# Kernel tuning notes

Hardware: AMD Instinct MI355X
Metric: run time of the kernel (lower is better)

Reference implementation:

```python
import jax, jax.numpy as jnp
import numpy as np

B, S, D, H, FF = 2, 1024, 1024, 16, 4096
EPS = 1e-6  # flax LayerNorm default


def _layernorm(x, scale, bias):
    m = jnp.mean(x, axis=-1, keepdims=True)
    v = jnp.mean(jnp.square(x - m), axis=-1, keepdims=True)
    return (x - m) * jax.lax.rsqrt(v + EPS) * scale + bias


def _attention(x, mask, w_qkv, b_qkv, w_o, b_o):
    # projection to 3*D, split into q,k,v
    p = x @ w_qkv + b_qkv                       # (B,S,3D)
    q, k, v = jnp.split(p, 3, axis=-1)          # each (B,S,D)
    hd = D // H
    # NOTE: faithful to source -- heads formed by a plain reshape of (B,S,D)
    qh = q.reshape(B, H, S, hd)
    kh = k.reshape(B, H, S, hd)
    vh = v.reshape(B, H, S, hd)
    # NOTE: scaled by sqrt(full hidden dim D), as in source (dim_key = key.shape[-1])
    scores = jnp.einsum('bhqd,bhkd->bhqk', qh, kh) / jnp.sqrt(jnp.asarray(D, x.dtype))
    scores = scores * mask                      # multiplicative mask (faithful)
    attn = jax.nn.softmax(scores, axis=-1)      # (B,H,S,S)
    ctx = jnp.einsum('bhqk,bhkd->bhqd', attn, vh).reshape(B, S, D)
    return ctx @ w_o + b_o, attn


def _geglu_ffn(x, w1, b1, wg, bg, w2, b2):
    h = x @ w1 + b1                              # (B,S,FF)
    g = h @ wg + bg                              # (B,S,2*FF)
    a, gate = g[..., :FF], g[..., FF:]
    tanh_res = jnp.tanh(gate * 0.7978845608 * (1 + 0.044715 * gate ** 2))
    act = a * 0.5 * gate * (1 + tanh_res)
    return act @ w2 + b2


def setup_inputs() -> dict:
    key = jax.random.key(0)
    ks = jax.random.split(key, 16)
    sc = 0.02
    inp = {
        'x': jax.random.normal(ks[0], (B, S, D), jnp.float32),
        'ln1_s': jnp.ones((D,), jnp.float32), 'ln1_b': jnp.zeros((D,), jnp.float32),
        'w_qkv1': jax.random.normal(ks[1], (D, 3 * D), jnp.float32) * sc,
        'b_qkv1': jnp.zeros((3 * D,), jnp.float32),
        'w_o1': jax.random.normal(ks[2], (D, D), jnp.float32) * sc,
        'b_o1': jnp.zeros((D,), jnp.float32),
        'ln2_s': jnp.ones((D,), jnp.float32), 'ln2_b': jnp.zeros((D,), jnp.float32),
        'w_qkv2': jax.random.normal(ks[3], (D, 3 * D), jnp.float32) * sc,
        'b_qkv2': jnp.zeros((3 * D,), jnp.float32),
        'w_o2': jax.random.normal(ks[4], (D, D), jnp.float32) * sc,
        'b_o2': jnp.zeros((D,), jnp.float32),
        'ln3_s': jnp.ones((D,), jnp.float32), 'ln3_b': jnp.zeros((D,), jnp.float32),
        'w1': jax.random.normal(ks[5], (D, FF), jnp.float32) * sc,
        'b1': jnp.zeros((FF,), jnp.float32),
        'wg': jax.random.normal(ks[6], (FF, 2 * FF), jnp.float32) * sc,
        'bg': jnp.zeros((2 * FF,), jnp.float32),
        'w2': jax.random.normal(ks[7], (FF, D), jnp.float32) * sc,
        'b2': jnp.zeros((D,), jnp.float32),
    }
    return inp


def reference(x, ln1_s, ln1_b, w_qkv1, b_qkv1, w_o1, b_o1,
              ln2_s, ln2_b, w_qkv2, b_qkv2, w_o2, b_o2,
              ln3_s, ln3_b, w1, b1, wg, bg, w2, b2):
    # causal mask: lower-triangular ones, multiplicative, broadcast over (B,H)
    mask = (jnp.arange(S)[:, None] >= jnp.arange(S)[None, :]).astype(jnp.int32)
    mask = jnp.broadcast_to(mask[None, None], (B, H, S, S))

    x = _layernorm(x, ln1_s, ln1_b)
    att1, attn_w1 = _attention(x, mask, w_qkv1, b_qkv1, w_o1, b_o1)
    x = x + att1                                  # dropout deterministic (identity)
    x = _layernorm(x, ln2_s, ln2_b)
    att2, attn_w2 = _attention(x, mask, w_qkv2, b_qkv2, w_o2, b_o2)
    x = x + att2
    x = _layernorm(x, ln3_s, ln3_b)
    out = _geglu_ffn(x, w1, b1, wg, bg, w2, b2)
    # NOTE: faithful to source -- final residual adds attention2 output
    x = out + att2
    return (x, attn_w1, attn_w2)
```

## Files before the change

### kernel.cpp

```cpp
#include <hip/hip_runtime.h>
#include <hip/hip_bf16.h>

#define B_ 2
#define S_ 1024
#define D_ 1024
#define H_ 16
#define HD_ 64
#define FF_ 4096
#define NROW_ (B_*S_)

typedef __hip_bfloat16 bf16;
typedef float f32x4 __attribute__((ext_vector_type(4)));
typedef int int4v __attribute__((ext_vector_type(4)));
typedef __bf16 bf16x8 __attribute__((ext_vector_type(8)));

__device__ __forceinline__ float bf2f(unsigned short u){
  return __uint_as_float((unsigned)u << 16);
}
__device__ __forceinline__ unsigned short f2bf(float f){
  unsigned u = __float_as_uint(f);
  return (unsigned short)((u + 0x7FFFu + ((u >> 16) & 1u)) >> 16);
}
__device__ __forceinline__ float gelu_gate(float a, float g){
  float t = tanhf(0.7978845608f * g * (1.f + 0.044715f * g * g));
  return a * 0.5f * g * (1.f + t);
}


__global__ __launch_bounds__(256) void tcvt(const float* __restrict__ W,
    unsigned short* __restrict__ Wt, int K, int N){
  __shared__ float tile[32][33];
  const int k0 = blockIdx.y*32, n0 = blockIdx.x*32;
  const int t = threadIdx.x;
  #pragma unroll
  for (int i = 0; i < 4; i++){
    int idx = t + i*256; int r = idx>>5, c = idx&31;
    tile[r][c] = W[(size_t)(k0+r)*N + n0 + c];
  }
  __syncthreads();
  #pragma unroll
  for (int i = 0; i < 4; i++){
    int idx = t + i*256; int r = idx>>5, c = idx&31;
    Wt[(size_t)(n0+r)*K + k0 + c] = f2bf(tile[c][r]);
  }
}

__global__ __launch_bounds__(256) void lnb_k(const float* __restrict__ x,
    const float* __restrict__ sc, const float* __restrict__ bi, unsigned short* __restrict__ y){
  const int row = blockIdx.x;
  const int t = threadIdx.x;
  const float* xr = x + (size_t)row * D_;
  float4 v = *(const float4*)&xr[t*4];
  __shared__ float red[8];
  float sum = v.x + v.y + v.z + v.w;
  #pragma unroll
  for (int o = 32; o > 0; o >>= 1) sum += __shfl_down(sum, o);
  if ((t & 63) == 0) red[t >> 6] = sum;
  __syncthreads();
  if (t == 0) red[4] = (red[0]+red[1]+red[2]+red[3]) * (1.f / D_);
  __syncthreads();
  const float mean = red[4];
  const float dx = v.x-mean, dy = v.y-mean, dz = v.z-mean, dw = v.w-mean;
  float sq = dx*dx + dy*dy + dz*dz + dw*dw;
  #pragma unroll
  for (int o = 32; o > 0; o >>= 1) sq += __shfl_down(sq, o);
  if ((t & 63) == 0) red[t >> 6] = sq;
  __syncthreads();
  if (t == 0) red[5] = (red[0]+red[1]+red[2]+red[3]) * (1.f / D_);
  __syncthreads();
  const float rstd = rsqrtf(red[5] + 1e-6f);
  float4 s4 = *(const float4*)&sc[t*4];
  float4 b4 = *(const float4*)&bi[t*4];
  ushort4 ov;
  ov.x = f2bf(dx*rstd*s4.x + b4.x);
  ov.y = f2bf(dy*rstd*s4.y + b4.y);
  ov.z = f2bf(dz*rstd*s4.z + b4.z);
  ov.w = f2bf(dw*rstd*s4.w + b4.w);
  *(ushort4*)&y[(size_t)row*D_ + t*4] = ov;
}

template<bool HAS_RES, bool RES_BF16, bool OUT_BF16>
__global__ __launch_bounds__(256) void mgemm(const unsigned short* __restrict__ A,
    const unsigned short* __restrict__ Bt, const float* __restrict__ bias,
    const void* __restrict__ res, void* __restrict__ Cv, int M, int N, int K){
  __shared__ unsigned short As[128*32];
  __shared__ unsigned short Bs[128*32];
  const int tid = threadIdx.x;
  const int bm = blockIdx.y*128, bn = blockIdx.x*128;
  const int lane = tid & 63, lq = lane >> 4, lr = lane & 15;
  const int wv = tid >> 6, wr = wv >> 1, wc = wv & 1;
  f32x4 acc[4][4] = {};
  int4v ra[2], rb[2];
  #pragma unroll
  for (int i = 0; i < 2; i++){
    int f = tid + i*256; int row = f>>2, s = f&3;
    ra[i] = *(const int4v*)&A[(size_t)(bm+row)*K + s*8];
    rb[i] = *(const int4v*)&Bt[(size_t)(bn+row)*K + s*8];
  }
  for (int k0 = 0; k0 < K; k0 += 32){
    __syncthreads();
    #pragma unroll
    for (int i = 0; i < 2; i++){
      int f = tid + i*256; int row = f>>2, s = f&3;
      int off = row*32 + ((s + (row>>1))&3)*8;
      *(int4v*)&As[off] = ra[i];
      *(int4v*)&Bs[off] = rb[i];
    }
    __syncthreads();
    if (k0 + 32 < K){
      #pragma unroll
      for (int i = 0; i < 2; i++){
        int f = tid + i*256; int row = f>>2, s = f&3;
        ra[i] = *(const int4v*)&A[(size_t)(bm+row)*K + k0+32 + s*8];
        rb[i] = *(const int4v*)&Bt[(size_t)(bn+row)*K + k0+32 + s*8];
      }
    }
    bf16x8 af[4], bfr[4];
    #pragma unroll
    for (int fm = 0; fm < 4; fm++){
      int r = wr*64 + fm*16 + lr;
      af[fm] = *(const bf16x8*)&As[r*32 + ((lq + (r>>1))&3)*8];
    }
    #pragma unroll
    for (int fn = 0; fn < 4; fn++){
      int r = wc*64 + fn*16 + lr;
      bfr[fn] = *(const bf16x8*)&Bs[r*32 + ((lq + (r>>1))&3)*8];
    }
    #pragma unroll
    for (int fm = 0; fm < 4; fm++)
      #pragma unroll
      for (int fn = 0; fn < 4; fn++)
        acc[fm][fn] = __builtin_amdgcn_mfma_f32_16x16x32_bf16(af[fm], bfr[fn], acc[fm][fn], 0, 0, 0);
  }
  #pragma unroll
  for (int fm = 0; fm < 4; fm++)
    #pragma unroll
    for (int fn = 0; fn < 4; fn++)
      #pragma unroll
      for (int rr = 0; rr < 4; rr++){
        int r = bm + wr*64 + fm*16 + lq*4 + rr;
        int c = bn + wc*64 + fn*16 + lr;
        size_t o = (size_t)r*N + c;
        float v = acc[fm][fn][rr] + bias[c];
        if (HAS_RES){
          if (RES_BF16) v += bf2f(((const unsigned short*)res)[o]);
          else          v += ((const float*)res)[o];
        }
        if (OUT_BF16) ((unsigned short*)Cv)[o] = f2bf(v);
        else          ((float*)Cv)[o] = v;
      }
}

__global__ __launch_bounds__(256) void mqkv(const unsigned short* __restrict__ A,
    const unsigned short* __restrict__ Bt, const float* __restrict__ bias,
    unsigned short* __restrict__ qh, unsigned short* __restrict__ kh, unsigned short* __restrict__ vt){
  const int K = D_;
  __shared__ unsigned short As[128*32];
  __shared__ unsigned short Bs[128*32];
  const int tid = threadIdx.x;
  const int bm = blockIdx.y*128, bn = blockIdx.x*128;
  const int lane = tid & 63, lq = lane >> 4, lr = lane & 15;
  const int wv = tid >> 6, wr = wv >> 1, wc = wv & 1;
  f32x4 acc[4][4] = {};
  int4v ra[2], rb[2];
  #pragma unroll
  for (int i = 0; i < 2; i++){
    int f = tid + i*256; int row = f>>2, s = f&3;
    ra[i] = *(const int4v*)&A[(size_t)(bm+row)*K + s*8];
    rb[i] = *(const int4v*)&Bt[(size_t)(bn+row)*K + s*8];
  }
  for (int k0 = 0; k0 < K; k0 += 32){
    __syncthreads();
    #pragma unroll
    for (int i = 0; i < 2; i++){
      int f = tid + i*256; int row = f>>2, s = f&3;
      int off = row*32 + ((s + (row>>1))&3)*8;
      *(int4v*)&As[off] = ra[i];
      *(int4v*)&Bs[off] = rb[i];
    }
    __syncthreads();
    if (k0 + 32 < K){
      #pragma unroll
      for (int i = 0; i < 2; i++){
        int f = tid + i*256; int row = f>>2, s = f&3;
        ra[i] = *(const int4v*)&A[(size_t)(bm+row)*K + k0+32 + s*8];
        rb[i] = *(const int4v*)&Bt[(size_t)(bn+row)*K + k0+32 + s*8];
      }
    }
    bf16x8 af[4], bfr[4];
    #pragma unroll
    for (int fm = 0; fm < 4; fm++){
      int r = wr*64 + fm*16 + lr;
      af[fm] = *(const bf16x8*)&As[r*32 + ((lq + (r>>1))&3)*8];
    }
    #pragma unroll
    for (int fn = 0; fn < 4; fn++){
      int r = wc*64 + fn*16 + lr;
      bfr[fn] = *(const bf16x8*)&Bs[r*32 + ((lq + (r>>1))&3)*8];
    }
    #pragma unroll
    for (int fm = 0; fm < 4; fm++)
      #pragma unroll
      for (int fn = 0; fn < 4; fn++)
        acc[fm][fn] = __builtin_amdgcn_mfma_f32_16x16x32_bf16(af[fm], bfr[fn], acc[fm][fn], 0, 0, 0);
  }
  #pragma unroll
  for (int fm = 0; fm < 4; fm++)
    #pragma unroll
    for (int fn = 0; fn < 4; fn++){
      int cbase = bn + wc*64 + fn*16 + lr;
      float bv = bias[cbase];
      if (cbase < 2*D_){
        unsigned short* dst = (cbase < D_) ? qh : kh;
        int cc = cbase & (D_-1);
        int u = cc >> 6, d2 = cc & 63;
        #pragma unroll
        for (int rr = 0; rr < 4; rr++){
          int r = bm + wr*64 + fm*16 + lq*4 + rr;
          int b = r >> 10, s = r & (S_-1);
          int h = s >> 6;
          int s2 = ((s & 63) << 4) + u;
          size_t off = (((size_t)(b*H_ + h))*S_ + s2)*HD_ + d2;
          dst[off] = f2bf(acc[fm][fn][rr] + bv);
        }
      } else {
        int cc = cbase - 2*D_;
        int u = cc >> 6, d2 = cc & 63;
        #pragma unroll
        for (int rr = 0; rr < 4; rr++){
          int r = bm + wr*64 + fm*16 + lq*4 + rr;
          int b = r >> 10, s = r & (S_-1);
          int h = s >> 6;
          int s2 = ((s & 63) << 4) + u;
          size_t off = (((size_t)(b*H_ + h))*HD_ + d2)*S_ + s2;
          vt[off] = f2bf(acc[fm][fn][rr] + bv);
        }
      }
    }
}

__global__ __launch_bounds__(256) void mgeglu(const unsigned short* __restrict__ A,
    const unsigned short* __restrict__ Wt, const float* __restrict__ bgp, unsigned short* __restrict__ act){
  const int K = FF_;
  __shared__ unsigned short As[128*32];
  __shared__ unsigned short Ba[64*32];
  __shared__ unsigned short Bg[64*32];
  const int tid = threadIdx.x;
  const int bm = blockIdx.y*128, bn = blockIdx.x*64;
  const int lane = tid & 63, lq = lane >> 4, lr = lane & 15;
  const int wv = tid >> 6, wr = wv >> 1, wc = wv & 1;
  f32x4 aa[4][2] = {};
  f32x4 ag[4][2] = {};
  int4v ra[2], rba, rbg;
  #pragma unroll
  for (int i = 0; i < 2; i++){
    int f = tid + i*256; int row = f>>2, s = f&3;
    ra[i] = *(const int4v*)&A[(size_t)(bm+row)*K + s*8];
  }
  { int row = tid>>2, s = tid&3;
    rba = *(const int4v*)&Wt[(size_t)(bn+row)*K + s*8];
    rbg = *(const int4v*)&Wt[(size_t)(FF_+bn+row)*K + s*8];
  }
  for (int k0 = 0; k0 < K; k0 += 32){
    __syncthreads();
    #pragma unroll
    for (int i = 0; i < 2; i++){
      int f = tid + i*256; int row = f>>2, s = f&3;
      *(int4v*)&As[row*32 + ((s + (row>>1))&3)*8] = ra[i];
    }
    { int row = tid>>2, s = tid&3;
      int off = row*32 + ((s + (row>>1))&3)*8;
      *(int4v*)&Ba[off] = rba;
      *(int4v*)&Bg[off] = rbg;
    }
    __syncthreads();
    if (k0 + 32 < K){
      #pragma unroll
      for (int i = 0; i < 2; i++){
        int f = tid + i*256; int row = f>>2, s = f&3;
        ra[i] = *(const int4v*)&A[(size_t)(bm+row)*K + k0+32 + s*8];
      }
      { int row = tid>>2, s = tid&3;
        rba = *(const int4v*)&Wt[(size_t)(bn+row)*K + k0+32 + s*8];
        rbg = *(const int4v*)&Wt[(size_t)(FF_+bn+row)*K + k0+32 + s*8];
      }
    }
    bf16x8 af[4], fa[2], fg[2];
    #pragma unroll
    for (int fm = 0; fm < 4; fm++){
      int r = wr*64 + fm*16 + lr;
      af[fm] = *(const bf16x8*)&As[r*32 + ((lq + (r>>1))&3)*8];
    }
    #pragma unroll
    for (int fn = 0; fn < 2; fn++){
      int r = wc*32 + fn*16 + lr;
      int off = r*32 + ((lq + (r>>1))&3)*8;
      fa[fn] = *(const bf16x8*)&Ba[off];
      fg[fn] = *(const bf16x8*)&Bg[off];
    }
    #pragma unroll
    for (int fm = 0; fm < 4; fm++)
      #pragma unroll
      for (int fn = 0; fn < 2; fn++){
        aa[fm][fn] = __builtin_amdgcn_mfma_f32_16x16x32_bf16(af[fm], fa[fn], aa[fm][fn], 0, 0, 0);
        ag[fm][fn] = __builtin_amdgcn_mfma_f32_16x16x32_bf16(af[fm], fg[fn], ag[fm][fn], 0, 0, 0);
      }
  }
  #pragma unroll
  for (int fm = 0; fm < 4; fm++)
    #pragma unroll
    for (int fn = 0; fn < 2; fn++)
      #pragma unroll
      for (int rr = 0; rr < 4; rr++){
        int r = bm + wr*64 + fm*16 + lq*4 + rr;
        int c = bn + wc*32 + fn*16 + lr;
        float a = aa[fm][fn][rr] + bgp[c];
        float g = ag[fm][fn][rr] + bgp[FF_ + c];
        act[(size_t)r*FF_ + c] = f2bf(gelu_gate(a, g));
      }
}

__global__ __launch_bounds__(256) void mstats(const unsigned short* __restrict__ qh,
    const unsigned short* __restrict__ kh, float2* __restrict__ stats){
  const int qt = blockIdx.x, bh = blockIdx.y;
  const int tid = threadIdx.x;
  const int lane = tid & 63, lq = lane >> 4, lr = lane & 15;
  const int wv = tid >> 6, wr = wv >> 1, wc = wv & 1;
  __shared__ unsigned short Qs[128*64];
  __shared__ unsigned short Ks[128*64];
  __shared__ float2 st[2][2][64];
  const unsigned short* Qp = qh + ((size_t)bh*S_ + qt*128)*HD_;
  #pragma unroll
  for (int i = 0; i < 4; i++){
    int f = tid + i*256;
    int row = f >> 3, s = f & 7;
    *(int4v*)&Qs[row*64 + ((s + row)&7)*8] = *(const int4v*)&Qp[(size_t)row*HD_ + s*8];
  }
  float m[4][4], l[4][4];
  #pragma unroll
  for (int fm = 0; fm < 4; fm++)
    #pragma unroll
    for (int rr = 0; rr < 4; rr++){ m[fm][rr] = -3.4e38f; l[fm][rr] = 0.f; }
  const int qg0 = qt*128;
  for (int kt = 0; kt <= qt; kt++){
    __syncthreads();
    const unsigned short* Kp = kh + ((size_t)bh*S_ + kt*128)*HD_;
    #pragma unroll
    for (int i = 0; i < 4; i++){
      int f = tid + i*256;
      int row = f >> 3, s = f & 7;
      *(int4v*)&Ks[row*64 + ((s + row)&7)*8] = *(const int4v*)&Kp[(size_t)row*HD_ + s*8];
    }
    __syncthreads();
    f32x4 acc[4][4] = {};
    #pragma unroll
    for (int ks = 0; ks < 2; ks++){
      bf16x8 af[4], bfr[4];
      #pragma unroll
      for (int fm = 0; fm < 4; fm++){
        int r = wr*64 + fm*16 + lr;
        af[fm] = *(const bf16x8*)&Qs[r*64 + ((ks*4+lq + r)&7)*8];
      }
      #pragma unroll
      for (int fn = 0; fn < 4; fn++){
        int r = wc*64 + fn*16 + lr;
        bfr[fn] = *(const bf16x8*)&Ks[r*64 + ((ks*4+lq + r)&7)*8];
      }
      #pragma unroll
      for (int fm = 0; fm < 4; fm++)
        #pragma unroll
        for (int fn = 0; fn < 4; fn++)
          acc[fm][fn] = __builtin_amdgcn_mfma_f32_16x16x32_bf16(af[fm], bfr[fn], acc[fm][fn], 0, 0, 0);
    }
    const int kg0 = kt*128;
    #pragma unroll
    for (int fm = 0; fm < 4; fm++)
      #pragma unroll
      for (int rr = 0; rr < 4; rr++){
        int r = wr*64 + fm*16 + lq*4 + rr;
        float v0 = (kg0 + wc*64 +  0 + lr <= qg0 + r) ? acc[fm][0][rr]*(1.f/32.f) : 0.f;
        float v1 = (kg0 + wc*64 + 16 + lr <= qg0 + r) ? acc[fm][1][rr]*(1.f/32.f) : 0.f;
        float v2 = (kg0 + wc*64 + 32 + lr <= qg0 + r) ? acc[fm][2][rr]*(1.f/32.f) : 0.f;
        float v3 = (kg0 + wc*64 + 48 + lr <= qg0 + r) ? acc[fm][3][rr]*(1.f/32.f) : 0.f;
        float tmax = fmaxf(fmaxf(v0,v1), fmaxf(v2,v3));
        tmax = fmaxf(tmax, __shfl_xor(tmax,1));
        tmax = fmaxf(tmax, __shfl_xor(tmax,2));
        tmax = fmaxf(tmax, __shfl_xor(tmax,4));
        tmax = fmaxf(tmax, __shfl_xor(tmax,8));
        float mn = fmaxf(m[fm][rr], tmax);
        float se = __expf(v0-mn)+__expf(v1-mn)+__expf(v2-mn)+__expf(v3-mn);
        se += __shfl_xor(se,1); se += __shfl_xor(se,2);
        se += __shfl_xor(se,4); se += __shfl_xor(se,8);
        l[fm][rr] = l[fm][rr]*__expf(m[fm][rr]-mn) + se;
        m[fm][rr] = mn;
      }
  }
  if (lr == 0){
    #pragma unroll
    for (int fm = 0; fm < 4; fm++)
      #pragma unroll
      for (int rr = 0; rr < 4; rr++){
        float2 v; v.x = m[fm][rr]; v.y = l[fm][rr];
        st[wr][wc][fm*16 + lq*4 + rr] = v;
      }
  }
  __syncthreads();
  if (wc == 0 && lr == 0){
    const float nz = (float)((7 - qt)*128);
    #pragma unroll
    for (int fm = 0; fm < 4; fm++)
      #pragma unroll
      for (int rr = 0; rr < 4; rr++){
        int r64 = fm*16 + lq*4 + rr;
        float2 a = st[wr][0][r64], b = st[wr][1][r64];
        float mf = fmaxf(a.x, b.x);
        float lf = a.y*__expf(a.x-mf) + b.y*__expf(b.x-mf);
        if (nz > 0.f){
          float mz = fmaxf(mf, 0.f);
          lf = lf*__expf(mf-mz) + nz*__expf(-mz);
          mf = mz;
        }
        float2 o; o.x = mf; o.y = lf;
        stats[(size_t)bh*S_ + qt*128 + wr*64 + r64] = o;
      }
  }
}

__global__ __launch_bounds__(256) void mpv(const unsigned short* __restrict__ qh,
    const unsigned short* __restrict__ kh, const unsigned short* __restrict__ vt,
    const float2* __restrict__ stats, float* __restrict__ attn, unsigned short* __restrict__ ctx){
  const int qt = blockIdx.x, bh = blockIdx.y;
  const int b = bh >> 4, h = bh & 15;
  const int tid = threadIdx.x;
  const int lane = tid & 63, lq = lane >> 4, lr = lane & 15;
  const int wv = tid >> 6, wr = wv >> 1, wc = wv & 1;
  __shared__ unsigned short Qs[128*64];
  __shared__ unsigned short Ks[128*64];
  __shared__ unsigned short Pt[128*128];
  __shared__ unsigned short Vt[64*128];
  const unsigned short* Qp = qh + ((size_t)bh*S_ + qt*128)*HD_;
  const unsigned short* Vp = vt + (size_t)bh*HD_*S_;
  float* Ap = attn + ((size_t)bh*S_ + qt*128)*S_;
  #pragma unroll
  for (int i = 0; i < 4; i++){
    int f = tid + i*256;
    int row = f >> 3, s = f & 7;
    *(int4v*)&Qs[row*64 + ((s + row)&7)*8] = *(const int4v*)&Qp[(size_t)row*HD_ + s*8];
  }
  float mS[4][4], lI[4][4];
  #pragma unroll
  for (int fm = 0; fm < 4; fm++)
    #pragma unroll
    for (int rr = 0; rr < 4; rr++){
      float2 s2 = stats[(size_t)bh*S_ + qt*128 + wr*64 + fm*16 + lq*4 + rr];
      mS[fm][rr] = s2.x; lI[fm][rr] = 1.f / s2.y;
    }
  const int qg0 = qt*128;
  f32x4 oacc[4][2] = {};
  for (int kt = 0; kt < 8; kt++){
    __syncthreads();
    #pragma unroll
    for (int i = 0; i < 4; i++){
      int f = tid + i*256;
      int row = f >> 4, s = f & 15;
      *(int4v*)&Vt[row*128 + ((s + row)&15)*8] = *(const int4v*)&Vp[(size_t)row*S_ + kt*128 + s*8];
    }
    if (kt <= qt){
      const unsigned short* Kp = kh + ((size_t)bh*S_ + kt*128)*HD_;
      #pragma unroll
      for (int i = 0; i < 4; i++){
        int f = tid + i*256;
        int row = f >> 3, s = f & 7;
        *(int4v*)&Ks[row*64 + ((s + row)&7)*8] = *(const int4v*)&Kp[(size_t)row*HD_ + s*8];
      }
      __syncthreads();
      f32x4 acc[4][4] = {};
      #pragma unroll
      for (int ks = 0; ks < 2; ks++){
        bf16x8 af[4], bfr[4];
        #pragma unroll
        for (int fm = 0; fm < 4; fm++){
          int r = wr*64 + fm*16 + lr;
          af[fm] = *(const bf16x8*)&Qs[r*64 + ((ks*4+lq + r)&7)*8];
        }
        #pragma unroll
        for (int fn = 0; fn < 4; fn++){
          int r = wc*64 + fn*16 + lr;
          bfr[fn] = *(const bf16x8*)&Ks[r*64 + ((ks*4+lq + r)&7)*8];
        }
        #pragma unroll
        for (int fm = 0; fm < 4; fm++)
          #pragma unroll
          for (int fn = 0; fn < 4; fn++)
            acc[fm][fn] = __builtin_amdgcn_mfma_f32_16x16x32_bf16(af[fm], bfr[fn], acc[fm][fn], 0, 0, 0);
      }
      const int kg0 = kt*128;
      #pragma unroll
      for (int fm = 0; fm < 4; fm++)
        #pragma unroll
        for (int fn = 0; fn < 4; fn++)
          #pragma unroll
          for (int rr = 0; rr < 4; rr++){
            int r = wr*64 + fm*16 + lq*4 + rr;
            int c = wc*64 + fn*16 + lr;
            float v = (kg0 + c <= qg0 + r) ? acc[fm][fn][rr]*(1.f/32.f) : 0.f;
            float p = __expf(v - mS[fm][rr]) * lI[fm][rr];
            Ap[(size_t)r*S_ + kg0 + c] = p;
            Pt[r*128 + (((c>>3) + r)&15)*8 + (c&7)] = f2bf(p);
          }
      __syncthreads();
    } else {
      __syncthreads();
      int rt = tid >> 1, hk = tid & 1;
      float2 srow = stats[(size_t)bh*S_ + qt*128 + rt];
      float p = __expf(-srow.x) * (1.f / srow.y);
      unsigned short pb = f2bf(p);
      int rep = (unsigned)pb | ((unsigned)pb << 16);
      int4v pv = {rep, rep, rep, rep};
      float4 pf = {p, p, p, p};
      #pragma unroll
      for (int sl = 0; sl < 8; sl++){
        int slot = hk*8 + sl;
        *(int4v*)&Pt[rt*128 + ((slot + rt)&15)*8] = pv;
        *(float4*)&Ap[(size_t)rt*S_ + kt*128 + hk*64 + sl*8] = pf;
        *(float4*)&Ap[(size_t)rt*S_ + kt*128 + hk*64 + sl*8 + 4] = pf;
      }
      __syncthreads();
    }
    #pragma unroll
    for (int ks = 0; ks < 4; ks++){
      bf16x8 af[4], bfv[2];
      #pragma unroll
      for (int fm = 0; fm < 4; fm++){
        int r = wr*64 + fm*16 + lr;
        af[fm] = *(const bf16x8*)&Pt[r*128 + ((ks*4+lq + r)&15)*8];
      }
      #pragma unroll
      for (int fn = 0; fn < 2; fn++){
        int r = wc*32 + fn*16 + lr;
        bfv[fn] = *(const bf16x8*)&Vt[r*128 + ((ks*4+lq + r)&15)*8];
      }
      #pragma unroll
      for (int fm = 0; fm < 4; fm++)
        #pragma unroll
        for (int fn = 0; fn < 2; fn++)
          oacc[fm][fn] = __builtin_amdgcn_mfma_f32_16x16x32_bf16(af[fm], bfv[fn], oacc[fm][fn], 0, 0, 0);
    }
  }
  #pragma unroll
  for (int fm = 0; fm < 4; fm++)
    #pragma unroll
    for (int fn = 0; fn < 2; fn++){
      int d = wc*32 + fn*16 + lr;
      #pragma unroll
      for (int rr = 0; rr < 4; rr++){
        int q = qt*128 + wr*64 + fm*16 + lq*4 + rr;
        size_t orow = ((size_t)b*S_ + h*HD_ + (q>>4)) * D_ + ((q&15)<<6) + d;
        ctx[orow] = f2bf(oacc[fm][fn][rr]);
      }
    }
}

__global__ __launch_bounds__(256) void addbf(const unsigned short* __restrict__ a,
    const float* __restrict__ b, float* __restrict__ c){
  size_t i = ((size_t)blockIdx.x*256 + threadIdx.x)*4;
  ushort4 av = *(const ushort4*)&a[i];
  float4 bv = *(const float4*)&b[i];
  float4 o = {bf2f(av.x)+bv.x, bf2f(av.y)+bv.y, bf2f(av.z)+bv.z, bf2f(av.w)+bv.w};
  *(float4*)&c[i] = o;
}


__global__ __launch_bounds__(256) void ln_kernel(const float* __restrict__ x,
    const float* __restrict__ sc, const float* __restrict__ bi, float* __restrict__ y){
  const int row = blockIdx.x;
  const int t = threadIdx.x;
  const float* xr = x + (size_t)row * D_;
  float4 v = *(const float4*)&xr[t*4];
  __shared__ float red[8];
  float sum = v.x + v.y + v.z + v.w;
  #pragma unroll
  for (int o = 32; o > 0; o >>= 1) sum += __shfl_down(sum, o);
  if ((t & 63) == 0) red[t >> 6] = sum;
  __syncthreads();
  if (t == 0) red[4] = (red[0]+red[1]+red[2]+red[3]) * (1.f / D_);
  __syncthreads();
  const float mean = red[4];
  const float dx = v.x-mean, dy = v.y-mean, dz = v.z-mean, dw = v.w-mean;
  float sq = dx*dx + dy*dy + dz*dz + dw*dw;
  #pragma unroll
  for (int o = 32; o > 0; o >>= 1) sq += __shfl_down(sq, o);
  if ((t & 63) == 0) red[t >> 6] = sq;
  __syncthreads();
  if (t == 0) red[5] = (red[0]+red[1]+red[2]+red[3]) * (1.f / D_);
  __syncthreads();
  const float rstd = rsqrtf(red[5] + 1e-6f);
  float4 s4 = *(const float4*)&sc[t*4];
  float4 b4 = *(const float4*)&bi[t*4];
  float4 o4;
  o4.x = dx*rstd*s4.x + b4.x;
  o4.y = dy*rstd*s4.y + b4.y;
  o4.z = dz*rstd*s4.z + b4.z;
  o4.w = dw*rstd*s4.w + b4.w;
  *(float4*)&y[(size_t)row*D_ + t*4] = o4;
}

__global__ __launch_bounds__(256) void gemm_qkv_kernel(const float* __restrict__ A,
    const float* __restrict__ W, const float* __restrict__ bias,
    float* __restrict__ qh, float* __restrict__ kh, float* __restrict__ vh){
  constexpr int BK=32;
  const int K = D_, N = 3*D_;
  __shared__ float As[BK][64+4];
  __shared__ float Bs[BK][64+4];
  const int bm = blockIdx.y*64, bn = blockIdx.x*64;
  const int tid = threadIdx.x;
  const int tx = tid & 15, ty = tid >> 4;
  float acc[4][4] = {};
  for (int k0 = 0; k0 < K; k0 += BK){
    #pragma unroll
    for (int i = 0; i < 2; i++){
      int idx = tid + i*256;
      int m = idx >> 3, kq = idx & 7;
      float4 v = *(const float4*)&A[(size_t)(bm+m)*K + k0 + kq*4];
      As[kq*4+0][m] = v.x; As[kq*4+1][m] = v.y;
      As[kq*4+2][m] = v.z; As[kq*4+3][m] = v.w;
    }
    #pragma unroll
    for (int i = 0; i < 2; i++){
      int idx = tid + i*256;
      int k = idx >> 4, nq = idx & 15;
      *(float4*)&Bs[k][nq*4] = *(const float4*)&W[(size_t)(k0+k)*N + bn + nq*4];
    }
    __syncthreads();
    #pragma unroll
    for (int kk = 0; kk < BK; kk++){
      float4 a4 = *(const float4*)&As[kk][ty*4];
      float4 b4 = *(const float4*)&Bs[kk][tx*4];
      float a[4] = {a4.x,a4.y,a4.z,a4.w};
      float b[4] = {b4.x,b4.y,b4.z,b4.w};
      #pragma unroll
      for (int i = 0; i < 4; i++)
        #pragma unroll
        for (int j = 0; j < 4; j++)
          acc[i][j] += a[i]*b[j];
    }
    __syncthreads();
  }
  float4 bias4 = *(const float4*)&bias[bn + tx*4];
  float* dst = (bn < D_) ? qh : (bn < 2*D_) ? kh : vh;
  const int c = (bn & (D_-1)) + tx*4;
  const int u = c >> 6;
  const int d2 = c & 63;
  #pragma unroll
  for (int i = 0; i < 4; i++){
    int r = bm + ty*4 + i;
    int b = r >> 10, s = r & (S_-1);
    int h = s >> 6;
    int s2 = ((s & 63) << 4) + u;
    size_t off = (((size_t)(b*H_ + h))*S_ + s2)*HD_ + d2;
    float4 o = {acc[i][0]+bias4.x, acc[i][1]+bias4.y, acc[i][2]+bias4.z, acc[i][3]+bias4.w};
    *(float4*)&dst[off] = o;
  }
}

__global__ __launch_bounds__(256) void attn_kernel(const float* __restrict__ qh,
    const float* __restrict__ kh, float* __restrict__ attn){
  const int q = blockIdx.x & (S_-1);
  const int bh = blockIdx.x >> 10;
  const int t = threadIdx.x;
  const float* qrow = qh + ((size_t)bh*S_ + q) * HD_;
  const float* Kp = kh + (size_t)bh*S_*HD_;
  __shared__ float qs[HD_];
  __shared__ float red[8];
  if (t < 16) ((float4*)qs)[t] = ((const float4*)qrow)[t];
  __syncthreads();
  float vals[4];
  float vmax = 0.f;
  #pragma unroll
  for (int j = 0; j < 4; j++){
    int k = t + j*256;
    float dot = 0.f;
    if (k <= q){
      const float4* Kr = (const float4*)&Kp[(size_t)k*HD_];
      #pragma unroll
      for (int dqi = 0; dqi < 16; dqi++){
        float4 kv = Kr[dqi];
        float4 qv = ((const float4*)qs)[dqi];
        dot += kv.x*qv.x + kv.y*qv.y + kv.z*qv.z + kv.w*qv.w;
      }
      dot *= (1.f/32.f);
    }
    vals[j] = dot;
    vmax = fmaxf(vmax, dot);
  }
  #pragma unroll
  for (int o = 32; o > 0; o >>= 1) vmax = fmaxf(vmax, __shfl_down(vmax, o));
  if ((t & 63) == 0) red[t >> 6] = vmax;
  __syncthreads();
  if (t == 0) red[4] = fmaxf(fmaxf(red[0],red[1]), fmaxf(red[2],red[3]));
  __syncthreads();
  const float m = red[4];
  float lsum = 0.f;
  #pragma unroll
  for (int j = 0; j < 4; j++){ vals[j] = __expf(vals[j]-m); lsum += vals[j]; }
  #pragma unroll
  for (int o = 32; o > 0; o >>= 1) lsum += __shfl_down(lsum, o);
  if ((t & 63) == 0) red[t >> 6] = lsum;
  __syncthreads();
  if (t == 0) red[5] = red[0]+red[1]+red[2]+red[3];
  __syncthreads();
  const float rinv = 1.f / red[5];
  float* arow = attn + ((size_t)bh*S_ + q) * S_;
  #pragma unroll
  for (int j = 0; j < 4; j++)
    arow[t + j*256] = vals[j] * rinv;
}

__global__ __launch_bounds__(256) void ctx_kernel(const float* __restrict__ attn,
    const float* __restrict__ vh, float* __restrict__ ctx){
  constexpr int BQ = 64, BK = 32;
  __shared__ float As[BK][BQ+4];
  __shared__ float Bs[BK][HD_+4];
  const int bh = blockIdx.y;
  const int b = bh >> 4, h = bh & 15;
  const int q0 = blockIdx.x * BQ;
  const float* Ap = attn + (size_t)bh*S_*S_;
  const float* Vp = vh + (size_t)bh*S_*HD_;
  const int tid = threadIdx.x;
  const int tx = tid & 15, ty = tid >> 4;
  float acc[4][4] = {};
  for (int k0 = 0; k0 < S_; k0 += BK){
    #pragma unroll
    for (int i = 0; i < 2; i++){
      int idx = tid + i*256;
      int m = idx >> 3, kq = idx & 7;
      float4 v = *(const float4*)&Ap[(size_t)(q0+m)*S_ + k0 + kq*4];
      As[kq*4+0][m] = v.x; As[kq*4+1][m] = v.y;
      As[kq*4+2][m] = v.z; As[kq*4+3][m] = v.w;
    }
    #pragma unroll
    for (int i = 0; i < 2; i++){
      int idx = tid + i*256;
      int k = idx >> 4, nq = idx & 15;
      *(float4*)&Bs[k][nq*4] = *(const float4*)&Vp[(size_t)(k0+k)*HD_ + nq*4];
    }
    __syncthreads();
    #pragma unroll
    for (int kk = 0; kk < BK; kk++){
      float4 a4 = *(const float4*)&As[kk][ty*4];
      float4 b4 = *(const float4*)&Bs[kk][tx*4];
      float a[4] = {a4.x,a4.y,a4.z,a4.w};
      float bb[4] = {b4.x,b4.y,b4.z,b4.w};
      #pragma unroll
      for (int i=0;i<4;i++)
        #pragma unroll
        for (int j=0;j<4;j++)
          acc[i][j] += a[i]*bb[j];
    }
    __syncthreads();
  }
  #pragma unroll
  for (int i = 0; i < 4; i++){
    int qq = q0 + ty*4 + i;
    size_t orow = ((size_t)b*S_ + h*HD_ + (qq>>4)) * D_ + ((qq&15)<<6) + tx*4;
    float4 o4 = {acc[i][0], acc[i][1], acc[i][2], acc[i][3]};
    *(float4*)&ctx[orow] = o4;
  }
}

template<bool A_BF16>
__global__ __launch_bounds__(256) void gemm_kernel(const void* __restrict__ Av,
    const float* __restrict__ W, const float* __restrict__ bias,
    const float* __restrict__ res, float* __restrict__ C,
    int M, int N, int K){
  constexpr int BK=32;
  __shared__ float As[BK][64+4];
  __shared__ float Bs[BK][64+4];
  const int bm = blockIdx.y*64, bn = blockIdx.x*64;
  const int tid = threadIdx.x;
  const int tx = tid & 15, ty = tid >> 4;
  float acc[4][4] = {};
  for (int k0 = 0; k0 < K; k0 += BK){
    #pragma unroll
    for (int i = 0; i < 2; i++){
      int idx = tid + i*256;
      int m = idx >> 3, kq = idx & 7;
      if (A_BF16){
        const unsigned short* A = (const unsigned short*)Av;
        ushort4 uu = *(const ushort4*)&A[(size_t)(bm+m)*K + k0 + kq*4];
        As[kq*4+0][m] = bf2f(uu.x); As[kq*4+1][m] = bf2f(uu.y);
        As[kq*4+2][m] = bf2f(uu.z); As[kq*4+3][m] = bf2f(uu.w);
      } else {
        const float* A = (const float*)Av;
        float4 v = *(const float4*)&A[(size_t)(bm+m)*K + k0 + kq*4];
        As[kq*4+0][m] = v.x; As[kq*4+1][m] = v.y;
        As[kq*4+2][m] = v.z; As[kq*4+3][m] = v.w;
      }
    }
    #pragma unroll
    for (int i = 0; i < 2; i++){
      int idx = tid + i*256;
      int k = idx >> 4, nq = idx & 15;
      *(float4*)&Bs[k][nq*4] = *(const float4*)&W[(size_t)(k0+k)*N + bn + nq*4];
    }
    __syncthreads();
    #pragma unroll
    for (int kk = 0; kk < BK; kk++){
      float4 a4 = *(const float4*)&As[kk][ty*4];
      float4 b4 = *(const float4*)&Bs[kk][tx*4];
      float a[4] = {a4.x,a4.y,a4.z,a4.w};
      float b[4] = {b4.x,b4.y,b4.z,b4.w};
      #pragma unroll
      for (int i = 0; i < 4; i++)
        #pragma unroll
        for (int j = 0; j < 4; j++)
          acc[i][j] += a[i]*b[j];
    }
    __syncthreads();
  }
  float4 bias4 = *(const float4*)&bias[bn + tx*4];
  #pragma unroll
  for (int i = 0; i < 4; i++){
    int r = bm + ty*4 + i;
    size_t base = (size_t)r*N + bn + tx*4;
    float c0 = acc[i][0] + bias4.x;
    float c1 = acc[i][1] + bias4.y;
    float c2 = acc[i][2] + bias4.z;
    float c3 = acc[i][3] + bias4.w;
    if (res){
      float4 r4 = *(const float4*)&res[base];
      c0 += r4.x; c1 += r4.y; c2 += r4.z; c3 += r4.w;
    }
    float4 o4 = {c0,c1,c2,c3};
    *(float4*)&C[base] = o4;
  }
}

__global__ __launch_bounds__(256) void gemm_geglu_kernel(const float* __restrict__ A,
    const float* __restrict__ W, const float* __restrict__ bgp, unsigned short* __restrict__ act){
  constexpr int BK=32;
  const int K = FF_, N = 2*FF_;
  __shared__ float As[BK][64+4];
  __shared__ float Ba[BK][64+4];
  __shared__ float Bg[BK][64+4];
  const int bm = blockIdx.y*64, bn = blockIdx.x*64;
  const int tid = threadIdx.x;
  const int tx = tid & 15, ty = tid >> 4;
  float acc_a[4][4] = {};
  float acc_g[4][4] = {};
  for (int k0 = 0; k0 < K; k0 += BK){
    #pragma unroll
    for (int i = 0; i < 2; i++){
      int idx = tid + i*256;
      int m = idx >> 3, kq = idx & 7;
      float4 v = *(const float4*)&A[(size_t)(bm+m)*K + k0 + kq*4];
      As[kq*4+0][m] = v.x; As[kq*4+1][m] = v.y;
      As[kq*4+2][m] = v.z; As[kq*4+3][m] = v.w;
    }
    #pragma unroll
    for (int i = 0; i < 2; i++){
      int idx = tid + i*256;
      int k = idx >> 4, nq = idx & 15;
      const float* Wr = &W[(size_t)(k0+k)*N];
      *(float4*)&Ba[k][nq*4] = *(const float4*)&Wr[bn + nq*4];
      *(float4*)&Bg[k][nq*4] = *(const float4*)&Wr[FF_ + bn + nq*4];
    }
    __syncthreads();
    #pragma unroll
    for (int kk = 0; kk < BK; kk++){
      float4 a4 = *(const float4*)&As[kk][ty*4];
      float4 p4 = *(const float4*)&Ba[kk][tx*4];
      float4 g4 = *(const float4*)&Bg[kk][tx*4];
      float a[4] = {a4.x,a4.y,a4.z,a4.w};
      float pa[4] = {p4.x,p4.y,p4.z,p4.w};
      float pg[4] = {g4.x,g4.y,g4.z,g4.w};
      #pragma unroll
      for (int i = 0; i < 4; i++)
        #pragma unroll
        for (int j = 0; j < 4; j++){
          acc_a[i][j] += a[i]*pa[j];
          acc_g[i][j] += a[i]*pg[j];
        }
    }
    __syncthreads();
  }
  float4 ba4 = *(const float4*)&bgp[bn + tx*4];
  float4 bg4 = *(const float4*)&bgp[FF_ + bn + tx*4];
  const float bav[4] = {ba4.x, ba4.y, ba4.z, ba4.w};
  const float bgv[4] = {bg4.x, bg4.y, bg4.z, bg4.w};
  #pragma unroll
  for (int i = 0; i < 4; i++){
    int r = bm + ty*4 + i;
    size_t base = (size_t)r*FF_ + bn + tx*4;
    act[base+0] = f2bf(gelu_gate(acc_a[i][0]+bav[0], acc_g[i][0]+bgv[0]));
    act[base+1] = f2bf(gelu_gate(acc_a[i][1]+bav[1], acc_g[i][1]+bgv[1]));
    act[base+2] = f2bf(gelu_gate(acc_a[i][2]+bav[2], acc_g[i][2]+bgv[2]));
    act[base+3] = f2bf(gelu_gate(acc_a[i][3]+bav[3], acc_g[i][3]+bgv[3]));
  }
}

__global__ __launch_bounds__(256) void add_kernel(const float* __restrict__ a,
    const float* __restrict__ b, float* __restrict__ c){
  size_t i = ((size_t)blockIdx.x*256 + threadIdx.x)*4;
  float4 x = *(const float4*)&a[i];
  float4 y = *(const float4*)&b[i];
  float4 o = {x.x+y.x, x.y+y.y, x.z+y.z, x.w+y.w};
  *(float4*)&c[i] = o;
}


extern "C" void kernel_launch(void* const* d_in, const int* in_sizes, int n_in,
                              void* d_out, int out_size, void* d_ws, size_t ws_size,
                              hipStream_t stream){
  const float* x0     = (const float*)d_in[0];
  const float* ln1_s  = (const float*)d_in[1];
  const float* ln1_b  = (const float*)d_in[2];
  const float* w_qkv1 = (const float*)d_in[3];
  const float* b_qkv1 = (const float*)d_in[4];
  const float* w_o1   = (const float*)d_in[5];
  const float* b_o1   = (const float*)d_in[6];
  const float* ln2_s  = (const float*)d_in[7];
  const float* ln2_b  = (const float*)d_in[8];
  const float* w_qkv2 = (const float*)d_in[9];
  const float* b_qkv2 = (const float*)d_in[10];
  const float* w_o2   = (const float*)d_in[11];
  const float* b_o2   = (const float*)d_in[12];
  const float* ln3_s  = (const float*)d_in[13];
  const float* ln3_b  = (const float*)d_in[14];
  const float* w1     = (const float*)d_in[15];
  const float* b1     = (const float*)d_in[16];
  const float* wg     = (const float*)d_in[17];
  const float* bg     = (const float*)d_in[18];
  const float* w2     = (const float*)d_in[19];
  const float* b2     = (const float*)d_in[20];

  const size_t MB_ = 1u<<20;
  const size_t FAST_NEED = 148*MB_;
  float* out_x = (float*)d_out;
  float* attn1 = out_x + 2*MB_;
  float* attn2 = attn1 + 32*MB_;
  dim3 blk(256);

  if (ws_size >= FAST_NEED){
    char* w8 = (char*)d_ws;
    float* att  = (float*)(w8 + 0);
    float* xcur = (float*)(w8 + 8*MB_);
    unsigned short* lnb     = (unsigned short*)(w8 + 16*MB_);
    unsigned short* wqkv1t  = (unsigned short*)(w8 + 20*MB_);
    unsigned short* wqkv2t  = (unsigned short*)(w8 + 26*MB_);
    unsigned short* wo1t    = (unsigned short*)(w8 + 32*MB_);
    unsigned short* wo2t    = (unsigned short*)(w8 + 34*MB_);
    unsigned short* w1t     = (unsigned short*)(w8 + 36*MB_);
    unsigned short* w2t     = (unsigned short*)(w8 + 44*MB_);
    unsigned short* wgt     = (unsigned short*)(w8 + 52*MB_);
    unsigned short* qhb     = (unsigned short*)(w8 + 116*MB_);
    unsigned short* khb     = (unsigned short*)(w8 + 120*MB_);
    unsigned short* vtb     = (unsigned short*)(w8 + 124*MB_);
    unsigned short* ctxb    = (unsigned short*)(w8 + 128*MB_);
    unsigned short* hbufb   = (unsigned short*)(w8 + 116*MB_);
    unsigned short* actb    = (unsigned short*)(w8 + 132*MB_);
    float2* stats           = (float2*)(w8 + 132*MB_);

    tcvt<<<dim3(96,32),  blk, 0, stream>>>(w_qkv1, wqkv1t, 1024, 3072);
    tcvt<<<dim3(96,32),  blk, 0, stream>>>(w_qkv2, wqkv2t, 1024, 3072);
    tcvt<<<dim3(32,32),  blk, 0, stream>>>(w_o1,   wo1t,   1024, 1024);
    tcvt<<<dim3(32,32),  blk, 0, stream>>>(w_o2,   wo2t,   1024, 1024);
    tcvt<<<dim3(128,32), blk, 0, stream>>>(w1,     w1t,    1024, 4096);
    tcvt<<<dim3(256,128),blk, 0, stream>>>(wg,     wgt,    4096, 8192);
    tcvt<<<dim3(32,128), blk, 0, stream>>>(w2,     w2t,    4096, 1024);
    lnb_k<<<NROW_, blk, 0, stream>>>(x0, ln1_s, ln1_b, lnb);
    mqkv<<<dim3(24,16), blk, 0, stream>>>(lnb, wqkv1t, b_qkv1, qhb, khb, vtb);
    mstats<<<dim3(8,32), blk, 0, stream>>>(qhb, khb, stats);
    mpv<<<dim3(8,32), blk, 0, stream>>>(qhb, khb, vtb, stats, attn1, ctxb);
    mgemm<true,true,false><<<dim3(8,16), blk, 0, stream>>>(ctxb, wo1t, b_o1, lnb, xcur, NROW_, D_, D_);
    lnb_k<<<NROW_, blk, 0, stream>>>(xcur, ln2_s, ln2_b, lnb);
    mqkv<<<dim3(24,16), blk, 0, stream>>>(lnb, wqkv2t, b_qkv2, qhb, khb, vtb);
    mstats<<<dim3(8,32), blk, 0, stream>>>(qhb, khb, stats);
    mpv<<<dim3(8,32), blk, 0, stream>>>(qhb, khb, vtb, stats, attn2, ctxb);
    mgemm<false,false,false><<<dim3(8,16), blk, 0, stream>>>(ctxb, wo2t, b_o2, nullptr, att, NROW_, D_, D_);
    addbf<<<2048, blk, 0, stream>>>(lnb, att, xcur);
    lnb_k<<<NROW_, blk, 0, stream>>>(xcur, ln3_s, ln3_b, lnb);
    mgemm<false,false,true><<<dim3(32,16), blk, 0, stream>>>(lnb, w1t, b1, nullptr, hbufb, NROW_, FF_, D_);
    mgeglu<<<dim3(64,16), blk, 0, stream>>>(hbufb, wgt, bg, actb);
    mgemm<true,false,false><<<dim3(8,16), blk, 0, stream>>>(actb, w2t, b2, att, out_x, NROW_, D_, FF_);
    return;
  }

  if (ws_size < (size_t)72*MB_) return;
  float* ws = (float*)d_ws;
  const size_t M1 = 1u<<20;
  float* att    = ws;
  float* xcur   = ws + 2*M1;
  float* ln_out = ws + 4*M1;
  float* qh     = ws + 6*M1;
  float* kh     = ws + 8*M1;
  float* vh     = ws + 10*M1;
  float* ctx    = ws + 12*M1;
  float* hbuf   = ws + 6*M1;
  unsigned short* actb = (unsigned short*)(ws + 14*M1);

  ln_kernel<<<NROW_, blk, 0, stream>>>(x0, ln1_s, ln1_b, ln_out);
  gemm_qkv_kernel<<<dim3(48,32), blk, 0, stream>>>(ln_out, w_qkv1, b_qkv1, qh, kh, vh);
  attn_kernel<<<B_*H_*S_, blk, 0, stream>>>(qh, kh, attn1);
  ctx_kernel<<<dim3(16, B_*H_), blk, 0, stream>>>(attn1, vh, ctx);
  gemm_kernel<false><<<dim3(16,32), blk, 0, stream>>>(ctx, w_o1, b_o1, ln_out, xcur, NROW_, D_, D_);
  ln_kernel<<<NROW_, blk, 0, stream>>>(xcur, ln2_s, ln2_b, ln_out);
  gemm_qkv_kernel<<<dim3(48,32), blk, 0, stream>>>(ln_out, w_qkv2, b_qkv2, qh, kh, vh);
  attn_kernel<<<B_*H_*S_, blk, 0, stream>>>(qh, kh, attn2);
  ctx_kernel<<<dim3(16, B_*H_), blk, 0, stream>>>(attn2, vh, ctx);
  gemm_kernel<false><<<dim3(16,32), blk, 0, stream>>>(ctx, w_o2, b_o2, nullptr, att, NROW_, D_, D_);
  add_kernel<<<2048, blk, 0, stream>>>(ln_out, att, xcur);
  ln_kernel<<<NROW_, blk, 0, stream>>>(xcur, ln3_s, ln3_b, ln_out);
  gemm_kernel<false><<<dim3(64,32), blk, 0, stream>>>(ln_out, w1, b1, nullptr, hbuf, NROW_, FF_, D_);
  gemm_geglu_kernel<<<dim3(64,32), blk, 0, stream>>>(hbuf, wg, bg, actb);
  gemm_kernel<true><<<dim3(16,32), blk, 0, stream>>>(actb, w2, b2, att, out_x, NROW_, D_, FF_);
}
```

Before: 669.9 us.

## Widen GEGLU tile, add XCD-aware block swizzle, merge weight conversions

```diff
diff --git a/kernel.cpp b/kernel.cpp
--- a/kernel.cpp
+++ b/kernel.cpp
@@ -25,12 +25,37 @@
   float t = tanhf(0.7978845608f * g * (1.f + 0.044715f * g * g));
   return a * 0.5f * g * (1.f + t);
 }
-
-
-__global__ __launch_bounds__(256) void tcvt(const float* __restrict__ W,
-    unsigned short* __restrict__ Wt, int K, int N){
+__device__ __forceinline__ void xcd_swz(int& bx, int& by){
+  int nx = gridDim.x, tot = nx * gridDim.y;
+  int flat = by * nx + bx;
+  int cpx = tot >> 3;
+  int w = (flat & 7) * cpx + (flat >> 3);
+  bx = w % nx; by = w / nx;
+}
+
+
+__global__ __launch_bounds__(256) void tcvt_all(
+    const float* __restrict__ w_qkv1, const float* __restrict__ w_qkv2,
+    const float* __restrict__ w_o1,   const float* __restrict__ w_o2,
+    const float* __restrict__ w1,     const float* __restrict__ wg,
+    const float* __restrict__ w2,
+    unsigned short* __restrict__ t_qkv1, unsigned short* __restrict__ t_qkv2,
+    unsigned short* __restrict__ t_o1,   unsigned short* __restrict__ t_o2,
+    unsigned short* __restrict__ t_w1,   unsigned short* __restrict__ t_wg,
+    unsigned short* __restrict__ t_w2){
   __shared__ float tile[32][33];
-  const int k0 = blockIdx.y*32, n0 = blockIdx.x*32;
+  int id = blockIdx.x;
+  const float* W; unsigned short* Wt; int K, N, t0;
+  if      (id <  3072){ W=w_qkv1; Wt=t_qkv1; K=1024; N=3072; t0=0; }
+  else if (id <  6144){ W=w_qkv2; Wt=t_qkv2; K=1024; N=3072; t0=3072; }
+  else if (id <  7168){ W=w_o1;   Wt=t_o1;   K=1024; N=1024; t0=6144; }
+  else if (id <  8192){ W=w_o2;   Wt=t_o2;   K=1024; N=1024; t0=7168; }
+  else if (id < 12288){ W=w1;     Wt=t_w1;   K=1024; N=4096; t0=8192; }
+  else if (id < 45056){ W=wg;     Wt=t_wg;   K=4096; N=8192; t0=12288; }
+  else               { W=w2;     Wt=t_w2;   K=4096; N=1024; t0=45056; }
+  int tl = id - t0;
+  int nx = N >> 5;
+  int n0 = (tl % nx) * 32, k0 = (tl / nx) * 32;
   const int t = threadIdx.x;
   #pragma unroll
   for (int i = 0; i < 4; i++){
@@ -86,7 +111,9 @@
   __shared__ unsigned short As[128*32];
   __shared__ unsigned short Bs[128*32];
   const int tid = threadIdx.x;
-  const int bm = blockIdx.y*128, bn = blockIdx.x*128;
+  int bx = blockIdx.x, by = blockIdx.y;
+  xcd_swz(bx, by);
+  const int bm = by*128, bn = bx*128;
   const int lane = tid & 63, lq = lane >> 4, lr = lane & 15;
   const int wv = tid >> 6, wr = wv >> 1, wc = wv & 1;
   f32x4 acc[4][4] = {};
@@ -158,7 +185,9 @@
   __shared__ unsigned short As[128*32];
   __shared__ unsigned short Bs[128*32];
   const int tid = threadIdx.x;
-  const int bm = blockIdx.y*128, bn = blockIdx.x*128;
+  int bx = blockIdx.x, by = blockIdx.y;
+  xcd_swz(bx, by);
+  const int bm = by*128, bn = bx*128;
   const int lane = tid & 63, lq = lane >> 4, lr = lane & 15;
   const int wv = tid >> 6, wr = wv >> 1, wc = wv & 1;
   f32x4 acc[4][4] = {};
@@ -243,57 +272,53 @@
     const unsigned short* __restrict__ Wt, const float* __restrict__ bgp, unsigned short* __restrict__ act){
   const int K = FF_;
   __shared__ unsigned short As[128*32];
-  __shared__ unsigned short Ba[64*32];
-  __shared__ unsigned short Bg[64*32];
+  __shared__ unsigned short Ba[128*32];
+  __shared__ unsigned short Bg[128*32];
   const int tid = threadIdx.x;
-  const int bm = blockIdx.y*128, bn = blockIdx.x*64;
+  int bx = blockIdx.x, by = blockIdx.y;
+  xcd_swz(bx, by);
+  const int bm = by*128, bn = bx*128;
   const int lane = tid & 63, lq = lane >> 4, lr = lane & 15;
   const int wv = tid >> 6, wr = wv >> 1, wc = wv & 1;
-  f32x4 aa[4][2] = {};
-  f32x4 ag[4][2] = {};
-  int4v ra[2], rba, rbg;
+  f32x4 aa[4][4] = {};
+  f32x4 ag[4][4] = {};
+  int4v ra[2], rba[2], rbg[2];
   #pragma unroll
   for (int i = 0; i < 2; i++){
     int f = tid + i*256; int row = f>>2, s = f&3;
-    ra[i] = *(const int4v*)&A[(size_t)(bm+row)*K + s*8];
-  }
-  { int row = tid>>2, s = tid&3;
-    rba = *(const int4v*)&Wt[(size_t)(bn+row)*K + s*8];
-    rbg = *(const int4v*)&Wt[(size_t)(FF_+bn+row)*K + s*8];
+    ra[i]  = *(const int4v*)&A [(size_t)(bm+row)*K + s*8];
+    rba[i] = *(const int4v*)&Wt[(size_t)(bn+row)*K + s*8];
+    rbg[i] = *(const int4v*)&Wt[(size_t)(FF_+bn+row)*K + s*8];
   }
   for (int k0 = 0; k0 < K; k0 += 32){
     __syncthreads();
     #pragma unroll
     for (int i = 0; i < 2; i++){
       int f = tid + i*256; int row = f>>2, s = f&3;
-      *(int4v*)&As[row*32 + ((s + (row>>1))&3)*8] = ra[i];
-    }
-    { int row = tid>>2, s = tid&3;
       int off = row*32 + ((s + (row>>1))&3)*8;
-      *(int4v*)&Ba[off] = rba;
-      *(int4v*)&Bg[off] = rbg;
+      *(int4v*)&As[off] = ra[i];
+      *(int4v*)&Ba[off] = rba[i];
+      *(int4v*)&Bg[off] = rbg[i];
     }
     __syncthreads();
     if (k0 + 32 < K){
       #pragma unroll
       for (int i = 0; i < 2; i++){
         int f = tid + i*256; int row = f>>2, s = f&3;
-        ra[i] = *(const int4v*)&A[(size_t)(bm+row)*K + k0+32 + s*8];
-      }
-      { int row = tid>>2, s = tid&3;
-        rba = *(const int4v*)&Wt[(size_t)(bn+row)*K + k0+32 + s*8];
-        rbg = *(const int4v*)&Wt[(size_t)(FF_+bn+row)*K + k0+32 + s*8];
-      }
-    }
-    bf16x8 af[4], fa[2], fg[2];
+        ra[i]  = *(const int4v*)&A [(size_t)(bm+row)*K + k0+32 + s*8];
+        rba[i] = *(const int4v*)&Wt[(size_t)(bn+row)*K + k0+32 + s*8];
+        rbg[i] = *(const int4v*)&Wt[(size_t)(FF_+bn+row)*K + k0+32 + s*8];
+      }
+    }
+    bf16x8 af[4], fa[4], fg[4];
     #pragma unroll
     for (int fm = 0; fm < 4; fm++){
       int r = wr*64 + fm*16 + lr;
       af[fm] = *(const bf16x8*)&As[r*32 + ((lq + (r>>1))&3)*8];
     }
     #pragma unroll
-    for (int fn = 0; fn < 2; fn++){
-      int r = wc*32 + fn*16 + lr;
+    for (int fn = 0; fn < 4; fn++){
+      int r = wc*64 + fn*16 + lr;
       int off = r*32 + ((lq + (r>>1))&3)*8;
       fa[fn] = *(const bf16x8*)&Ba[off];
       fg[fn] = *(const bf16x8*)&Bg[off];
@@ -301,7 +326,7 @@
     #pragma unroll
     for (int fm = 0; fm < 4; fm++)
       #pragma unroll
-      for (int fn = 0; fn < 2; fn++){
+      for (int fn = 0; fn < 4; fn++){
         aa[fm][fn] = __builtin_amdgcn_mfma_f32_16x16x32_bf16(af[fm], fa[fn], aa[fm][fn], 0, 0, 0);
         ag[fm][fn] = __builtin_amdgcn_mfma_f32_16x16x32_bf16(af[fm], fg[fn], ag[fm][fn], 0, 0, 0);
       }
@@ -309,11 +334,11 @@
   #pragma unroll
   for (int fm = 0; fm < 4; fm++)
     #pragma unroll
-    for (int fn = 0; fn < 2; fn++)
+    for (int fn = 0; fn < 4; fn++)
       #pragma unroll
       for (int rr = 0; rr < 4; rr++){
         int r = bm + wr*64 + fm*16 + lq*4 + rr;
-        int c = bn + wc*32 + fn*16 + lr;
+        int c = bn + wc*64 + fn*16 + lr;
         float a = aa[fm][fn][rr] + bgp[c];
         float g = ag[fm][fn][rr] + bgp[FF_ + c];
         act[(size_t)r*FF_ + c] = f2bf(gelu_gate(a, g));
@@ -322,7 +347,8 @@
 
 __global__ __launch_bounds__(256) void mstats(const unsigned short* __restrict__ qh,
     const unsigned short* __restrict__ kh, float2* __restrict__ stats){
-  const int qt = blockIdx.x, bh = blockIdx.y;
+  int qt = blockIdx.x, bh = blockIdx.y;
+  xcd_swz(qt, bh);
   const int tid = threadIdx.x;
   const int lane = tid & 63, lq = lane >> 4, lr = lane & 15;
   const int wv = tid >> 6, wr = wv >> 1, wc = wv & 1;
@@ -429,7 +455,8 @@
 __global__ __launch_bounds__(256) void mpv(const unsigned short* __restrict__ qh,
     const unsigned short* __restrict__ kh, const unsigned short* __restrict__ vt,
     const float2* __restrict__ stats, float* __restrict__ attn, unsigned short* __restrict__ ctx){
-  const int qt = blockIdx.x, bh = blockIdx.y;
+  int qt = blockIdx.x, bh = blockIdx.y;
+  xcd_swz(qt, bh);
   const int b = bh >> 4, h = bh & 15;
   const int tid = threadIdx.x;
   const int lane = tid & 63, lq = lane >> 4, lr = lane & 15;
@@ -961,13 +988,8 @@
     unsigned short* actb    = (unsigned short*)(w8 + 132*MB_);
     float2* stats           = (float2*)(w8 + 132*MB_);
 
-    tcvt<<<dim3(96,32),  blk, 0, stream>>>(w_qkv1, wqkv1t, 1024, 3072);
-    tcvt<<<dim3(96,32),  blk, 0, stream>>>(w_qkv2, wqkv2t, 1024, 3072);
-    tcvt<<<dim3(32,32),  blk, 0, stream>>>(w_o1,   wo1t,   1024, 1024);
-    tcvt<<<dim3(32,32),  blk, 0, stream>>>(w_o2,   wo2t,   1024, 1024);
-    tcvt<<<dim3(128,32), blk, 0, stream>>>(w1,     w1t,    1024, 4096);
-    tcvt<<<dim3(256,128),blk, 0, stream>>>(wg,     wgt,    4096, 8192);
-    tcvt<<<dim3(32,128), blk, 0, stream>>>(w2,     w2t,    4096, 1024);
+    tcvt_all<<<49152, blk, 0, stream>>>(w_qkv1, w_qkv2, w_o1, w_o2, w1, wg, w2,
+                                        wqkv1t, wqkv2t, wo1t, wo2t, w1t, wgt, w2t);
     lnb_k<<<NROW_, blk, 0, stream>>>(x0, ln1_s, ln1_b, lnb);
     mqkv<<<dim3(24,16), blk, 0, stream>>>(lnb, wqkv1t, b_qkv1, qhb, khb, vtb);
     mstats<<<dim3(8,32), blk, 0, stream>>>(qhb, khb, stats);
@@ -981,7 +1003,7 @@
     addbf<<<2048, blk, 0, stream>>>(lnb, att, xcur);
     lnb_k<<<NROW_, blk, 0, stream>>>(xcur, ln3_s, ln3_b, lnb);
     mgemm<false,false,true><<<dim3(32,16), blk, 0, stream>>>(lnb, w1t, b1, nullptr, hbufb, NROW_, FF_, D_);
-    mgeglu<<<dim3(64,16), blk, 0, stream>>>(hbufb, wgt, bg, actb);
+    mgeglu<<<dim3(32,16), blk, 0, stream>>>(hbufb, wgt, bg, actb);
     mgemm<true,false,false><<<dim3(8,16), blk, 0, stream>>>(actb, w2t, b2, att, out_x, NROW_, D_, FF_);
     return;
   }
```

After: 706.1 us. 1.05x slower.
